# Kernel optimization log

Hardware: AMD Instinct MI355X
Metric: run time of the kernel (lower is better)

Reference implementation:

```python
import jax, jax.numpy as jnp
import numpy as np

B, T, E = 2, 2048, 1024
H, D = 16, 64          # num_heads, head_dim (v_head_dim == head_dim)


def setup_inputs() -> dict:
    key = jax.random.key(0)
    ks = jax.random.split(key, 10)
    s = lambda fan_in: 1.0 / np.sqrt(fan_in)
    inp = {
        "embed": jax.random.normal(ks[0], (B, T, E), dtype=jnp.float32),
        "mask": jax.random.randint(ks[1], (B, T, T), 0, 2) > 0,
        # Linear weights stored as [in, out] (y = x @ W + b)
        "Wq": jax.random.uniform(ks[2], (E, H * D), minval=-s(E), maxval=s(E)),
        "bq": jnp.zeros((H * D,), jnp.float32),
        "Wk": jax.random.uniform(ks[3], (E, H * D), minval=-s(E), maxval=s(E)),
        "bk": jnp.zeros((H * D,), jnp.float32),
        "Wv": jax.random.uniform(ks[4], (E, H * D), minval=-s(E), maxval=s(E)),
        "bv": jnp.zeros((H * D,), jnp.float32),
        "Wz": jax.random.uniform(ks[5], (H * D, E), minval=-s(H * D), maxval=s(H * D)),
        "bz": jnp.zeros((E,), jnp.float32),
    }
    return inp


def reference(embed, mask, Wq, bq, Wk, bk, Wv, bv, Wz, bz):
    # Self-attention: context = embed
    q = (embed @ Wq + bq).reshape(B, T, H, D)   # b t h d
    k = (embed @ Wk + bk).reshape(B, T, H, D)   # b T h d
    v = (embed @ Wv + bv).reshape(B, T, H, D)   # b T h d

    scale = D ** (-0.5)
    score = jnp.einsum('bthd,bThd->bhtT', q, k) * scale   # [b,h,t,T] materialized, as in source
    max_neg = -jnp.finfo(score.dtype).max
    score = jnp.where(mask[:, None, :, :], score, max_neg)
    norm_score = jax.nn.softmax(score, axis=-1)
    z = jnp.einsum('bhtT,bThd->bthd', norm_score, v)      # [b,t,h,d]
    flat_z = z.reshape(B, T, H * D)
    return flat_z @ Wz + bz
```

## Files before the change

### kernel.cpp

```cpp
#include <hip/hip_runtime.h>
#include <hip/hip_bf16.h>


typedef __bf16 bf8_t  __attribute__((ext_vector_type(8)));
typedef __bf16 bf4_t  __attribute__((ext_vector_type(4)));
typedef float  f4_t   __attribute__((ext_vector_type(4)));

constexpr int Bb = 2, Tt = 2048, Hh = 16, Dd = 64;

#define ASYNC16(g, l)                                                        \
    __builtin_amdgcn_global_load_lds(                                        \
        (const __attribute__((address_space(1))) void*)(g),                  \
        (__attribute__((address_space(3))) void*)(l), 16, 0, 0)

#if __has_builtin(__builtin_amdgcn_exp2f)
#define EXP2F(x) __builtin_amdgcn_exp2f(x)
#else
#define EXP2F(x) exp2f(x)
#endif

__global__ __launch_bounds__(256) void convert_kernel(
    const float* __restrict__ in, __bf16* __restrict__ out)
{
    int i = (blockIdx.x * 256 + threadIdx.x) * 4;
    float4 v = *reinterpret_cast<const float4*>(in + i);
    bf4_t o = {(__bf16)v.x, (__bf16)v.y, (__bf16)v.z, (__bf16)v.w};
    *reinterpret_cast<bf4_t*>(out + i) = o;
}

__global__ __launch_bounds__(256) void transpose_kernel(
    const float* __restrict__ w0, const float* __restrict__ w1,
    const float* __restrict__ w2, const float* __restrict__ w3,
    __bf16* __restrict__ o0, __bf16* __restrict__ o1,
    __bf16* __restrict__ o2, __bf16* __restrict__ o3)
{
    const float* in; __bf16* out;
    switch (blockIdx.z) {
        case 0: in = w0; out = o0; break;
        case 1: in = w1; out = o1; break;
        case 2: in = w2; out = o2; break;
        default: in = w3; out = o3; break;
    }
    __shared__ float t[32][33];
    int x  = threadIdx.x & 31;
    int y0 = threadIdx.x >> 5;
    int bx = blockIdx.x * 32;
    int by = blockIdx.y * 32;
    #pragma unroll
    for (int i = 0; i < 4; i++) {
        int y = y0 + i * 8;
        t[y][x] = in[(size_t)(by + y) * 1024 + bx + x];
    }
    __syncthreads();
    #pragma unroll
    for (int i = 0; i < 4; i++) {
        int y = y0 + i * 8;
        out[(size_t)(bx + y) * 1024 + by + x] = (__bf16)t[x][y];
    }
}

template <int TM, typename OutT>
__device__ __forceinline__ void gemm_body(const __bf16* __restrict__ A,
                                          const __bf16* __restrict__ Bt,
                                          const float* __restrict__ bias,
                                          OutT* __restrict__ out,
                                          int mode, float oscale, int bx, int by)
{
    constexpr int NI = TM / 32;
    alignas(16) __shared__ __bf16 As[TM * 64];
    alignas(16) __shared__ __bf16 Bs[128 * 64];

    int tid  = threadIdx.x;
    int lane = tid & 63;
    int quad = lane >> 4;
    int l16  = lane & 15;
    int wave = tid >> 6;
    int wm   = wave >> 1, wn = wave & 1;

    f4_t acc[NI][4];
    #pragma unroll
    for (int i = 0; i < NI; i++)
        #pragma unroll
        for (int j = 0; j < 4; j++)
            acc[i][j] = f4_t{0.f, 0.f, 0.f, 0.f};

    for (int kt = 0; kt < 1024; kt += 64) {
        #pragma unroll
        for (int i = 0; i < TM / 32; i++) {
            int c   = tid + 256 * i;
            int row = c >> 3, j = c & 7;
            ASYNC16(A + (size_t)(by * TM + row) * 1024 + kt + ((j ^ (row & 7)) * 8),
                    &As[c * 8]);
        }
        #pragma unroll
        for (int i = 0; i < 4; i++) {
            int c   = tid + 256 * i;
            int row = c >> 3, j = c & 7;
            ASYNC16(Bt + (size_t)(bx * 128 + row) * 1024 + kt + ((j ^ (row & 7)) * 8),
                    &Bs[c * 8]);
        }
        __syncthreads();

        bf8_t af[2][NI], bfr[2][4];
        #pragma unroll
        for (int c = 0; c < 2; c++) {
            #pragma unroll
            for (int im = 0; im < NI; im++) {
                int row = wm * (TM / 2) + im * 16 + l16;
                af[c][im] = *reinterpret_cast<const bf8_t*>(
                    &As[row * 64 + (((c * 4 + quad) ^ (row & 7)) * 8)]);
            }
            #pragma unroll
            for (int in_ = 0; in_ < 4; in_++) {
                int row = wn * 64 + in_ * 16 + l16;
                bfr[c][in_] = *reinterpret_cast<const bf8_t*>(
                    &Bs[row * 64 + (((c * 4 + quad) ^ (row & 7)) * 8)]);
            }
        }
        #pragma unroll
        for (int c = 0; c < 2; c++)
            #pragma unroll
            for (int im = 0; im < NI; im++)
                #pragma unroll
                for (int in_ = 0; in_ < 4; in_++)
                    acc[im][in_] = __builtin_amdgcn_mfma_f32_16x16x32_bf16(
                        af[c][im], bfr[c][in_], acc[im][in_], 0, 0, 0);
        __syncthreads();
    }

    #pragma unroll
    for (int im = 0; im < NI; im++) {
        #pragma unroll
        for (int in_ = 0; in_ < 4; in_++) {
            int gc  = bx * 128 + wn * 64 + in_ * 16 + l16;
            float bb = bias[gc];
            int gr0 = by * TM + wm * (TM / 2) + im * 16 + quad * 4;
            if (mode == 2) {
                int b = gr0 >> 11, t0 = gr0 & 2047;
                int h = gc >> 6,  d = gc & 63;
                bf4_t ov;
                #pragma unroll
                for (int r = 0; r < 4; r++)
                    ov[r] = (__bf16)(acc[im][in_][r] + bb);
                *reinterpret_cast<bf4_t*>(
                    (__bf16*)out + ((size_t)(b * Hh + h) * Dd + d) * Tt + t0) = ov;
            } else {
                #pragma unroll
                for (int r = 0; r < 4; r++) {
                    int gr  = gr0 + r;
                    float v = (acc[im][in_][r] + bb) * oscale;
                    size_t idx;
                    if (mode == 0) {
                        idx = (size_t)gr * 1024 + gc;
                    } else {
                        int b = gr >> 11, t = gr & 2047;
                        int h = gc >> 6,  d = gc & 63;
                        idx = ((size_t)(b * Hh + h) * Tt + t) * Dd + d;
                    }
                    out[idx] = (OutT)v;
                }
            }
        }
    }
}

__global__ __launch_bounds__(256) void gemm_qkv_kernel(
    const __bf16* __restrict__ A,
    const __bf16* __restrict__ WqT, const __bf16* __restrict__ WkT, const __bf16* __restrict__ WvT,
    const float* __restrict__ bq,  const float* __restrict__ bk,  const float* __restrict__ bv,
    __bf16* __restrict__ Qo, __bf16* __restrict__ Ko, __bf16* __restrict__ Vo)
{
    const __bf16* Bt; const float* bias; __bf16* out; int mode; float sc;
    if      (blockIdx.z == 0) { Bt = WqT; bias = bq; out = Qo; mode = 1; sc = 0.18033688011112042f; }
    else if (blockIdx.z == 1) { Bt = WkT; bias = bk; out = Ko; mode = 1; sc = 1.f; }
    else                      { Bt = WvT; bias = bv; out = Vo; mode = 2; sc = 1.f; }
    gemm_body<128, __bf16>(A, Bt, bias, out, mode, sc, blockIdx.x, blockIdx.y);
}

__global__ __launch_bounds__(256) void gemm_out_kernel(
    const __bf16* __restrict__ A, const __bf16* __restrict__ Bt,
    const float* __restrict__ bias, float* __restrict__ out)
{
    gemm_body<64, float>(A, Bt, bias, out, 0, 1.f, blockIdx.x, blockIdx.y);
}

__global__ __launch_bounds__(512, 4) void flash_kernel(
    const __bf16* __restrict__ Qb, const __bf16* __restrict__ Kb,
    const __bf16* __restrict__ Vb, const int* __restrict__ mask,
    __bf16* __restrict__ Zb)
{
    alignas(16) __shared__ __bf16 Ks[2][64 * 64];
    alignas(16) __shared__ __bf16 Vs[2][64 * 64];
    alignas(16) __shared__ __bf16 Ps[8 * 16 * 72];

    int tid  = threadIdx.x;
    int lane = tid & 63;
    int wave = tid >> 6;
    int quad = lane >> 4;
    int l16  = lane & 15;
    int b = blockIdx.z, h = blockIdx.y;
    int bh = b * Hh + h;
    int qrow = blockIdx.x * 128 + wave * 16;

    int srow = tid >> 3, sj = tid & 7;
    const __bf16* kgp = Kb + ((size_t)bh * Tt + srow) * Dd + ((sj ^ (srow & 7)) * 8);
    const __bf16* vgp = Vb + ((size_t)bh * Dd + srow) * Tt + ((sj ^ (srow & 7)) * 8);
    const int sdst = tid * 8;

    bf8_t qf[2];
    #pragma unroll
    for (int c = 0; c < 2; c++)
        qf[c] = *reinterpret_cast<const bf8_t*>(
            Qb + ((size_t)bh * Tt + qrow + l16) * Dd + c * 32 + quad * 8);

    const int* mp = mask + ((size_t)b * Tt + qrow + l16) * Tt + quad * 4;

    float l_i = 0.f;
    f4_t o[4];
    #pragma unroll
    for (int d = 0; d < 4; d++) o[d] = f4_t{0.f, 0.f, 0.f, 0.f};

    __bf16* pw = Ps + wave * 16 * 72;

    bf8_t kreg = *reinterpret_cast<const bf8_t*>(kgp);
    bf8_t vreg = *reinterpret_cast<const bf8_t*>(vgp);
    int4 ireg[4];
    #pragma unroll
    for (int n = 0; n < 4; n++)
        ireg[n] = *reinterpret_cast<const int4*>(mp + n * 16);

    for (int kt = 0; kt < Tt; kt += 64) {
        int par = (kt >> 6) & 1;
        *reinterpret_cast<bf8_t*>(&Ks[par][sdst]) = kreg;
        *reinterpret_cast<bf8_t*>(&Vs[par][sdst]) = vreg;
        f4_t s[4];
        #pragma unroll
        for (int n = 0; n < 4; n++)
            s[n] = f4_t{ireg[n].x ? 0.f : -1e30f, ireg[n].y ? 0.f : -1e30f,
                        ireg[n].z ? 0.f : -1e30f, ireg[n].w ? 0.f : -1e30f};
        __syncthreads();

        int ktn = (kt + 64 < Tt) ? kt + 64 : 0;
        kreg = *reinterpret_cast<const bf8_t*>(kgp + (size_t)ktn * Dd);
        vreg = *reinterpret_cast<const bf8_t*>(vgp + ktn);
        #pragma unroll
        for (int n = 0; n < 4; n++)
            ireg[n] = *reinterpret_cast<const int4*>(mp + ktn + n * 16);

        #pragma unroll
        for (int c = 0; c < 2; c++)
            #pragma unroll
            for (int n = 0; n < 4; n++) {
                int krow = n * 16 + l16;
                bf8_t kf = *reinterpret_cast<const bf8_t*>(
                    &Ks[par][krow * 64 + (((c * 4 + quad) ^ (krow & 7)) * 8)]);
                s[n] = __builtin_amdgcn_mfma_f32_16x16x32_bf16(kf, qf[c], s[n], 0, 0, 0);
            }

        float rs = 0.f;
        #pragma unroll
        for (int n = 0; n < 4; n++) {
            bf4_t pv4;
            #pragma unroll
            for (int r = 0; r < 4; r++) {
                float p = EXP2F(s[n][r]);
                rs += p;
                pv4[r] = (__bf16)p;
            }
            *reinterpret_cast<bf4_t*>(&pw[l16 * 72 + n * 16 + quad * 4]) = pv4;
        }
        rs += __shfl_xor(rs, 16);
        rs += __shfl_xor(rs, 32);
        l_i += rs;

        #pragma unroll
        for (int c = 0; c < 2; c++) {
            bf8_t pf = *reinterpret_cast<const bf8_t*>(
                &pw[l16 * 72 + c * 32 + quad * 8]);
            #pragma unroll
            for (int ds = 0; ds < 4; ds++) {
                int vrow = ds * 16 + l16;
                bf8_t vf = *reinterpret_cast<const bf8_t*>(
                    &Vs[par][vrow * 64 + (((c * 4 + quad) ^ (vrow & 7)) * 8)]);
                o[ds] = __builtin_amdgcn_mfma_f32_16x16x32_bf16(vf, pf, o[ds], 0, 0, 0);
            }
        }
    }

    float inv = 1.f / fmaxf(l_i, 1e-30f);
    size_t zrow = ((size_t)b * Tt + qrow + l16) * 1024 + h * 64;
    #pragma unroll
    for (int ds = 0; ds < 4; ds++) {
        bf4_t ov;
        #pragma unroll
        for (int r = 0; r < 4; r++) ov[r] = (__bf16)(o[ds][r] * inv);
        *reinterpret_cast<bf4_t*>(Zb + zrow + ds * 16 + quad * 4) = ov;
    }
}

extern "C" void kernel_launch(void* const* d_in, const int* in_sizes, int n_in,
                              void* d_out, int out_size, void* d_ws, size_t ws_size,
                              hipStream_t stream)
{
    (void)in_sizes; (void)n_in; (void)out_size; (void)ws_size;

    const float* embed = (const float*)d_in[0];
    const int*   mask  = (const int*)d_in[1];
    const float* Wq = (const float*)d_in[2];
    const float* bq = (const float*)d_in[3];
    const float* Wk = (const float*)d_in[4];
    const float* bk = (const float*)d_in[5];
    const float* Wv = (const float*)d_in[6];
    const float* bv = (const float*)d_in[7];
    const float* Wz = (const float*)d_in[8];
    const float* bz = (const float*)d_in[9];
    float* out = (float*)d_out;

    char* ws = (char*)d_ws;
    const size_t MB = (size_t)1024 * 1024;
    __bf16* WqT = (__bf16*)(ws + 0 * MB);
    __bf16* WkT = (__bf16*)(ws + 2 * MB);
    __bf16* WvT = (__bf16*)(ws + 4 * MB);
    __bf16* WzT = (__bf16*)(ws + 6 * MB);
    __bf16* Eb  = (__bf16*)(ws + 8 * MB);
    __bf16* Qb  = (__bf16*)(ws + 16 * MB);
    __bf16* Kb  = (__bf16*)(ws + 24 * MB);
    __bf16* Vb  = (__bf16*)(ws + 32 * MB);
    __bf16* Zb  = (__bf16*)(ws + 40 * MB);

    convert_kernel<<<dim3(4096), 256, 0, stream>>>(embed, Eb);
    transpose_kernel<<<dim3(32, 32, 4), 256, 0, stream>>>(Wq, Wk, Wv, Wz,
                                                          WqT, WkT, WvT, WzT);
    gemm_qkv_kernel<<<dim3(8, 32, 3), 256, 0, stream>>>(Eb, WqT, WkT, WvT,
                                                        bq, bk, bv, Qb, Kb, Vb);
    flash_kernel<<<dim3(16, Hh, Bb), 512, 0, stream>>>(Qb, Kb, Vb, mask, Zb);
    gemm_out_kernel<<<dim3(8, 64, 1), 256, 0, stream>>>(Zb, WzT, bz, out);
}
```

Before: 238.2 us.

## Process two query tiles per wave in flash attention to reuse K/V fragments

The flash kernel now runs 4 waves per block instead of 8, with each wave handling 32 query rows as two 16-row groups. Each K and V fragment read from LDS is reused for two MFMAs, halving LDS fragment traffic per unit of compute. The mask bias is also converted to bf16 at load time, so it is held in fewer registers. The trade-off is more accumulator registers per wave and fewer waves per block to hide latency.

```diff
diff --git a/kernel.cpp b/kernel.cpp
--- a/kernel.cpp
+++ b/kernel.cpp
@@ -184,14 +184,14 @@
     gemm_body<64, float>(A, Bt, bias, out, 0, 1.f, blockIdx.x, blockIdx.y);
 }
 
-__global__ __launch_bounds__(512, 4) void flash_kernel(
+__global__ __launch_bounds__(256, 2) void flash_kernel(
     const __bf16* __restrict__ Qb, const __bf16* __restrict__ Kb,
     const __bf16* __restrict__ Vb, const int* __restrict__ mask,
     __bf16* __restrict__ Zb)
 {
     alignas(16) __shared__ __bf16 Ks[2][64 * 64];
     alignas(16) __shared__ __bf16 Vs[2][64 * 64];
-    alignas(16) __shared__ __bf16 Ps[8 * 16 * 72];
+    alignas(16) __shared__ __bf16 Ps[4 * 2 * 16 * 72];
 
     int tid  = threadIdx.x;
     int lane = tid & 63;
@@ -200,52 +200,78 @@
     int l16  = lane & 15;
     int b = blockIdx.z, h = blockIdx.y;
     int bh = b * Hh + h;
-    int qrow = blockIdx.x * 128 + wave * 16;
-
-    int srow = tid >> 3, sj = tid & 7;
-    const __bf16* kgp = Kb + ((size_t)bh * Tt + srow) * Dd + ((sj ^ (srow & 7)) * 8);
-    const __bf16* vgp = Vb + ((size_t)bh * Dd + srow) * Tt + ((sj ^ (srow & 7)) * 8);
-    const int sdst = tid * 8;
-
-    bf8_t qf[2];
-    #pragma unroll
-    for (int c = 0; c < 2; c++)
-        qf[c] = *reinterpret_cast<const bf8_t*>(
-            Qb + ((size_t)bh * Tt + qrow + l16) * Dd + c * 32 + quad * 8);
-
-    const int* mp = mask + ((size_t)b * Tt + qrow + l16) * Tt + quad * 4;
-
-    float l_i = 0.f;
-    f4_t o[4];
-    #pragma unroll
-    for (int d = 0; d < 4; d++) o[d] = f4_t{0.f, 0.f, 0.f, 0.f};
-
-    __bf16* pw = Ps + wave * 16 * 72;
-
-    bf8_t kreg = *reinterpret_cast<const bf8_t*>(kgp);
-    bf8_t vreg = *reinterpret_cast<const bf8_t*>(vgp);
-    int4 ireg[4];
-    #pragma unroll
-    for (int n = 0; n < 4; n++)
-        ireg[n] = *reinterpret_cast<const int4*>(mp + n * 16);
+    int qbase = blockIdx.x * 128 + wave * 32;
+
+    int r0 = tid >> 3,        j0 = tid & 7;
+    int r1 = (tid + 256) >> 3, j1 = tid & 7;
+    const __bf16* kgp0 = Kb + ((size_t)bh * Tt + r0) * Dd + ((j0 ^ (r0 & 7)) * 8);
+    const __bf16* kgp1 = Kb + ((size_t)bh * Tt + r1) * Dd + ((j1 ^ (r1 & 7)) * 8);
+    const __bf16* vgp0 = Vb + ((size_t)bh * Dd + r0) * Tt + ((j0 ^ (r0 & 7)) * 8);
+    const __bf16* vgp1 = Vb + ((size_t)bh * Dd + r1) * Tt + ((j1 ^ (r1 & 7)) * 8);
+
+    bf8_t qf[2][2];
+    #pragma unroll
+    for (int qg = 0; qg < 2; qg++)
+        #pragma unroll
+        for (int c = 0; c < 2; c++)
+            qf[qg][c] = *reinterpret_cast<const bf8_t*>(
+                Qb + ((size_t)bh * Tt + qbase + qg * 16 + l16) * Dd + c * 32 + quad * 8);
+
+    const int* mp0 = mask + ((size_t)b * Tt + qbase + l16) * Tt + quad * 4;
+    const int* mp1 = mp0 + (size_t)16 * Tt;
+
+    float l_i[2] = {0.f, 0.f};
+    f4_t o[2][4];
+    #pragma unroll
+    for (int qg = 0; qg < 2; qg++)
+        #pragma unroll
+        for (int d = 0; d < 4; d++) o[qg][d] = f4_t{0.f, 0.f, 0.f, 0.f};
+
+    __bf16* pw0 = Ps + (wave * 2 + 0) * 16 * 72;
+    __bf16* pw1 = Ps + (wave * 2 + 1) * 16 * 72;
+
+    bf8_t kreg0 = *reinterpret_cast<const bf8_t*>(kgp0);
+    bf8_t kreg1 = *reinterpret_cast<const bf8_t*>(kgp1);
+    bf8_t vreg0 = *reinterpret_cast<const bf8_t*>(vgp0);
+    bf8_t vreg1 = *reinterpret_cast<const bf8_t*>(vgp1);
+    bf4_t breg[2][4];
+    #pragma unroll
+    for (int n = 0; n < 4; n++) {
+        int4 i0 = *reinterpret_cast<const int4*>(mp0 + n * 16);
+        int4 i1 = *reinterpret_cast<const int4*>(mp1 + n * 16);
+        const __bf16 z = (__bf16)0.f, neg = (__bf16)(-1e30f);
+        breg[0][n] = bf4_t{i0.x ? z : neg, i0.y ? z : neg, i0.z ? z : neg, i0.w ? z : neg};
+        breg[1][n] = bf4_t{i1.x ? z : neg, i1.y ? z : neg, i1.z ? z : neg, i1.w ? z : neg};
+    }
 
     for (int kt = 0; kt < Tt; kt += 64) {
         int par = (kt >> 6) & 1;
-        *reinterpret_cast<bf8_t*>(&Ks[par][sdst]) = kreg;
-        *reinterpret_cast<bf8_t*>(&Vs[par][sdst]) = vreg;
-        f4_t s[4];
-        #pragma unroll
-        for (int n = 0; n < 4; n++)
-            s[n] = f4_t{ireg[n].x ? 0.f : -1e30f, ireg[n].y ? 0.f : -1e30f,
-                        ireg[n].z ? 0.f : -1e30f, ireg[n].w ? 0.f : -1e30f};
+        *reinterpret_cast<bf8_t*>(&Ks[par][tid * 8])         = kreg0;
+        *reinterpret_cast<bf8_t*>(&Ks[par][(tid + 256) * 8]) = kreg1;
+        *reinterpret_cast<bf8_t*>(&Vs[par][tid * 8])         = vreg0;
+        *reinterpret_cast<bf8_t*>(&Vs[par][(tid + 256) * 8]) = vreg1;
+        f4_t s[2][4];
+        #pragma unroll
+        for (int qg = 0; qg < 2; qg++)
+            #pragma unroll
+            for (int n = 0; n < 4; n++)
+                s[qg][n] = f4_t{(float)breg[qg][n][0], (float)breg[qg][n][1],
+                                (float)breg[qg][n][2], (float)breg[qg][n][3]};
         __syncthreads();
 
         int ktn = (kt + 64 < Tt) ? kt + 64 : 0;
-        kreg = *reinterpret_cast<const bf8_t*>(kgp + (size_t)ktn * Dd);
-        vreg = *reinterpret_cast<const bf8_t*>(vgp + ktn);
-        #pragma unroll
-        for (int n = 0; n < 4; n++)
-            ireg[n] = *reinterpret_cast<const int4*>(mp + ktn + n * 16);
+        kreg0 = *reinterpret_cast<const bf8_t*>(kgp0 + (size_t)ktn * Dd);
+        kreg1 = *reinterpret_cast<const bf8_t*>(kgp1 + (size_t)ktn * Dd);
+        vreg0 = *reinterpret_cast<const bf8_t*>(vgp0 + ktn);
+        vreg1 = *reinterpret_cast<const bf8_t*>(vgp1 + ktn);
+        #pragma unroll
+        for (int n = 0; n < 4; n++) {
+            int4 i0 = *reinterpret_cast<const int4*>(mp0 + ktn + n * 16);
+            int4 i1 = *reinterpret_cast<const int4*>(mp1 + ktn + n * 16);
+            const __bf16 z = (__bf16)0.f, neg = (__bf16)(-1e30f);
+            breg[0][n] = bf4_t{i0.x ? z : neg, i0.y ? z : neg, i0.z ? z : neg, i0.w ? z : neg};
+            breg[1][n] = bf4_t{i1.x ? z : neg, i1.y ? z : neg, i1.z ? z : neg, i1.w ? z : neg};
+        }
 
         #pragma unroll
         for (int c = 0; c < 2; c++)
@@ -254,47 +280,56 @@
                 int krow = n * 16 + l16;
                 bf8_t kf = *reinterpret_cast<const bf8_t*>(
                     &Ks[par][krow * 64 + (((c * 4 + quad) ^ (krow & 7)) * 8)]);
-                s[n] = __builtin_amdgcn_mfma_f32_16x16x32_bf16(kf, qf[c], s[n], 0, 0, 0);
-            }
-
-        float rs = 0.f;
-        #pragma unroll
-        for (int n = 0; n < 4; n++) {
-            bf4_t pv4;
-            #pragma unroll
-            for (int r = 0; r < 4; r++) {
-                float p = EXP2F(s[n][r]);
-                rs += p;
-                pv4[r] = (__bf16)p;
-            }
-            *reinterpret_cast<bf4_t*>(&pw[l16 * 72 + n * 16 + quad * 4]) = pv4;
-        }
-        rs += __shfl_xor(rs, 16);
-        rs += __shfl_xor(rs, 32);
-        l_i += rs;
+                s[0][n] = __builtin_amdgcn_mfma_f32_16x16x32_bf16(kf, qf[0][c], s[0][n], 0, 0, 0);
+                s[1][n] = __builtin_amdgcn_mfma_f32_16x16x32_bf16(kf, qf[1][c], s[1][n], 0, 0, 0);
+            }
+
+        #pragma unroll
+        for (int qg = 0; qg < 2; qg++) {
+            __bf16* pw = qg ? pw1 : pw0;
+            float rs = 0.f;
+            #pragma unroll
+            for (int n = 0; n < 4; n++) {
+                bf4_t pv4;
+                #pragma unroll
+                for (int r = 0; r < 4; r++) {
+                    float p = EXP2F(s[qg][n][r]);
+                    rs += p;
+                    pv4[r] = (__bf16)p;
+                }
+                *reinterpret_cast<bf4_t*>(&pw[l16 * 72 + n * 16 + quad * 4]) = pv4;
+            }
+            rs += __shfl_xor(rs, 16);
+            rs += __shfl_xor(rs, 32);
+            l_i[qg] += rs;
+        }
 
         #pragma unroll
         for (int c = 0; c < 2; c++) {
-            bf8_t pf = *reinterpret_cast<const bf8_t*>(
-                &pw[l16 * 72 + c * 32 + quad * 8]);
+            bf8_t pf0 = *reinterpret_cast<const bf8_t*>(&pw0[l16 * 72 + c * 32 + quad * 8]);
+            bf8_t pf1 = *reinterpret_cast<const bf8_t*>(&pw1[l16 * 72 + c * 32 + quad * 8]);
             #pragma unroll
             for (int ds = 0; ds < 4; ds++) {
                 int vrow = ds * 16 + l16;
                 bf8_t vf = *reinterpret_cast<const bf8_t*>(
                     &Vs[par][vrow * 64 + (((c * 4 + quad) ^ (vrow & 7)) * 8)]);
-                o[ds] = __builtin_amdgcn_mfma_f32_16x16x32_bf16(vf, pf, o[ds], 0, 0, 0);
-            }
-        }
-    }
-
-    float inv = 1.f / fmaxf(l_i, 1e-30f);
-    size_t zrow = ((size_t)b * Tt + qrow + l16) * 1024 + h * 64;
-    #pragma unroll
-    for (int ds = 0; ds < 4; ds++) {
-        bf4_t ov;
-        #pragma unroll
-        for (int r = 0; r < 4; r++) ov[r] = (__bf16)(o[ds][r] * inv);
-        *reinterpret_cast<bf4_t*>(Zb + zrow + ds * 16 + quad * 4) = ov;
+                o[0][ds] = __builtin_amdgcn_mfma_f32_16x16x32_bf16(vf, pf0, o[0][ds], 0, 0, 0);
+                o[1][ds] = __builtin_amdgcn_mfma_f32_16x16x32_bf16(vf, pf1, o[1][ds], 0, 0, 0);
+            }
+        }
+    }
+
+    #pragma unroll
+    for (int qg = 0; qg < 2; qg++) {
+        float inv = 1.f / fmaxf(l_i[qg], 1e-30f);
+        size_t zrow = ((size_t)b * Tt + qbase + qg * 16 + l16) * 1024 + h * 64;
+        #pragma unroll
+        for (int ds = 0; ds < 4; ds++) {
+            bf4_t ov;
+            #pragma unroll
+            for (int r = 0; r < 4; r++) ov[r] = (__bf16)(o[qg][ds][r] * inv);
+            *reinterpret_cast<bf4_t*>(Zb + zrow + ds * 16 + quad * 4) = ov;
+        }
     }
 }
 
@@ -333,6 +368,6 @@
                                                           WqT, WkT, WvT, WzT);
     gemm_qkv_kernel<<<dim3(8, 32, 3), 256, 0, stream>>>(Eb, WqT, WkT, WvT,
                                                         bq, bk, bv, Qb, Kb, Vb);
-    flash_kernel<<<dim3(16, Hh, Bb), 512, 0, stream>>>(Qb, Kb, Vb, mask, Zb);
+    flash_kernel<<<dim3(16, Hh, Bb), 256, 0, stream>>>(Qb, Kb, Vb, mask, Zb);
     gemm_out_kernel<<<dim3(8, 64, 1), 256, 0, stream>>>(Zb, WzT, bz, out);
 }
```

After: 298.9 us. 25.5% more time.

## Split flash attention over two key halves and combine partials

Applied to the files above, without the earlier changes.

Splits the key/value sequence into two halves handled by separate blocks, which doubles the flash grid from 512 to 1024 blocks. Each block writes unnormalized fp32 partial outputs and row sums, and a new combine kernel adds them and normalizes into bf16. The occupancy hint rises to 6 blocks per CU. The aim is better CU utilization on the 256-CU device. The cost is an extra kernel launch plus roughly 32MB of fp32 partial writes and reads. Combining without a max correction is valid only because the scores carry no running-max subtraction (Q is pre-scaled and exp2 is used directly).

```diff
diff --git a/kernel.cpp b/kernel.cpp
--- a/kernel.cpp
+++ b/kernel.cpp
@@ -184,10 +184,10 @@
     gemm_body<64, float>(A, Bt, bias, out, 0, 1.f, blockIdx.x, blockIdx.y);
 }
 
-__global__ __launch_bounds__(512, 4) void flash_kernel(
+__global__ __launch_bounds__(512, 6) void flash_kernel(
     const __bf16* __restrict__ Qb, const __bf16* __restrict__ Kb,
     const __bf16* __restrict__ Vb, const int* __restrict__ mask,
-    __bf16* __restrict__ Zb)
+    float* __restrict__ Opart, float* __restrict__ Lpart)
 {
     alignas(16) __shared__ __bf16 Ks[2][64 * 64];
     alignas(16) __shared__ __bf16 Vs[2][64 * 64];
@@ -198,13 +198,16 @@
     int wave = tid >> 6;
     int quad = lane >> 4;
     int l16  = lane & 15;
-    int b = blockIdx.z, h = blockIdx.y;
-    int bh = b * Hh + h;
+    int b    = blockIdx.z >> 1;
+    int split= blockIdx.z & 1;
+    int h    = blockIdx.y;
+    int bh   = b * Hh + h;
     int qrow = blockIdx.x * 128 + wave * 16;
+    const int kt0 = split * 1024;
 
     int srow = tid >> 3, sj = tid & 7;
-    const __bf16* kgp = Kb + ((size_t)bh * Tt + srow) * Dd + ((sj ^ (srow & 7)) * 8);
-    const __bf16* vgp = Vb + ((size_t)bh * Dd + srow) * Tt + ((sj ^ (srow & 7)) * 8);
+    const __bf16* kgp = Kb + ((size_t)bh * Tt + kt0 + srow) * Dd + ((sj ^ (srow & 7)) * 8);
+    const __bf16* vgp = Vb + ((size_t)bh * Dd + srow) * Tt + kt0 + ((sj ^ (srow & 7)) * 8);
     const int sdst = tid * 8;
 
     bf8_t qf[2];
@@ -213,7 +216,7 @@
         qf[c] = *reinterpret_cast<const bf8_t*>(
             Qb + ((size_t)bh * Tt + qrow + l16) * Dd + c * 32 + quad * 8);
 
-    const int* mp = mask + ((size_t)b * Tt + qrow + l16) * Tt + quad * 4;
+    const int* mp = mask + ((size_t)b * Tt + qrow + l16) * Tt + kt0 + quad * 4;
 
     float l_i = 0.f;
     f4_t o[4];
@@ -229,7 +232,7 @@
     for (int n = 0; n < 4; n++)
         ireg[n] = *reinterpret_cast<const int4*>(mp + n * 16);
 
-    for (int kt = 0; kt < Tt; kt += 64) {
+    for (int kt = 0; kt < 1024; kt += 64) {
         int par = (kt >> 6) & 1;
         *reinterpret_cast<bf8_t*>(&Ks[par][sdst]) = kreg;
         *reinterpret_cast<bf8_t*>(&Vs[par][sdst]) = vreg;
@@ -240,7 +243,7 @@
                         ireg[n].z ? 0.f : -1e30f, ireg[n].w ? 0.f : -1e30f};
         __syncthreads();
 
-        int ktn = (kt + 64 < Tt) ? kt + 64 : 0;
+        int ktn = (kt + 64 < 1024) ? kt + 64 : 0;
         kreg = *reinterpret_cast<const bf8_t*>(kgp + (size_t)ktn * Dd);
         vreg = *reinterpret_cast<const bf8_t*>(vgp + ktn);
         #pragma unroll
@@ -287,15 +290,30 @@
         }
     }
 
-    float inv = 1.f / fmaxf(l_i, 1e-30f);
-    size_t zrow = ((size_t)b * Tt + qrow + l16) * 1024 + h * 64;
-    #pragma unroll
-    for (int ds = 0; ds < 4; ds++) {
-        bf4_t ov;
-        #pragma unroll
-        for (int r = 0; r < 4; r++) ov[r] = (__bf16)(o[ds][r] * inv);
-        *reinterpret_cast<bf4_t*>(Zb + zrow + ds * 16 + quad * 4) = ov;
-    }
+    size_t orow = ((size_t)(split * Bb + b) * Tt + qrow + l16) * 1024 + h * 64;
+    #pragma unroll
+    for (int ds = 0; ds < 4; ds++)
+        *reinterpret_cast<f4_t*>(Opart + orow + ds * 16 + quad * 4) = o[ds];
+    if (quad == 0)
+        Lpart[((size_t)(split * Bb + b) * Tt + qrow + l16) * Hh + h] = l_i;
+}
+
+__global__ __launch_bounds__(256) void combine_kernel(
+    const float* __restrict__ Opart, const float* __restrict__ Lpart,
+    __bf16* __restrict__ Zb)
+{
+    const size_t NTOT = (size_t)Bb * Tt * 1024;
+    size_t i = ((size_t)blockIdx.x * 256 + threadIdx.x) * 4;
+    size_t row = i >> 10;
+    int    h   = (int)((i & 1023) >> 6);
+    f4_t a = *reinterpret_cast<const f4_t*>(Opart + i);
+    f4_t c = *reinterpret_cast<const f4_t*>(Opart + NTOT + i);
+    float l = Lpart[row * Hh + h] + Lpart[(size_t)Bb * Tt * Hh + row * Hh + h];
+    float inv = 1.f / fmaxf(l, 1e-30f);
+    bf4_t ov;
+    #pragma unroll
+    for (int r = 0; r < 4; r++) ov[r] = (__bf16)((a[r] + c[r]) * inv);
+    *reinterpret_cast<bf4_t*>(Zb + i) = ov;
 }
 
 extern "C" void kernel_launch(void* const* d_in, const int* in_sizes, int n_in,
@@ -327,12 +345,15 @@
     __bf16* Kb  = (__bf16*)(ws + 24 * MB);
     __bf16* Vb  = (__bf16*)(ws + 32 * MB);
     __bf16* Zb  = (__bf16*)(ws + 40 * MB);
+    float*  Op  = (float*)(ws + 64 * MB);
+    float*  Lp  = (float*)(ws + 96 * MB);
 
     convert_kernel<<<dim3(4096), 256, 0, stream>>>(embed, Eb);
     transpose_kernel<<<dim3(32, 32, 4), 256, 0, stream>>>(Wq, Wk, Wv, Wz,
                                                           WqT, WkT, WvT, WzT);
     gemm_qkv_kernel<<<dim3(8, 32, 3), 256, 0, stream>>>(Eb, WqT, WkT, WvT,
                                                         bq, bk, bv, Qb, Kb, Vb);
-    flash_kernel<<<dim3(16, Hh, Bb), 512, 0, stream>>>(Qb, Kb, Vb, mask, Zb);
+    flash_kernel<<<dim3(16, Hh, Bb * 2), 512, 0, stream>>>(Qb, Kb, Vb, mask, Op, Lp);
+    combine_kernel<<<dim3(4096), 256, 0, stream>>>(Op, Lp, Zb);
     gemm_out_kernel<<<dim3(8, 64, 1), 256, 0, stream>>>(Zb, WzT, bz, out);
 }
```

Result: slower. 250.0 us (+4.9%).

## Fuse embed conversion into QKV GEMM and register-prefetch double-buffered GEMM tiles

Applied to the files above, without the earlier changes.

Removes the separate fp32->bf16 conversion kernel for the embeddings; the QKV GEMM now reads fp32 embed directly and converts in registers while staging to LDS. Both GEMMs switch from async global->LDS loads with two barriers per k-step to a register-prefetch scheme with double-buffered shared memory and one barrier per step, issuing the next tile's global loads before the MFMA work. Launch bounds now request two blocks per SM. In exchange, the QKV GEMM reads twice as many bytes of A per tile, uses more registers for the prefetch buffers, and doubles LDS use.

```diff
diff --git a/kernel.cpp b/kernel.cpp
--- a/kernel.cpp
+++ b/kernel.cpp
@@ -7,26 +7,12 @@
 typedef float  f4_t   __attribute__((ext_vector_type(4)));
 
 constexpr int Bb = 2, Tt = 2048, Hh = 16, Dd = 64;
-
-#define ASYNC16(g, l)                                                        \
-    __builtin_amdgcn_global_load_lds(                                        \
-        (const __attribute__((address_space(1))) void*)(g),                  \
-        (__attribute__((address_space(3))) void*)(l), 16, 0, 0)
 
 #if __has_builtin(__builtin_amdgcn_exp2f)
 #define EXP2F(x) __builtin_amdgcn_exp2f(x)
 #else
 #define EXP2F(x) exp2f(x)
 #endif
-
-__global__ __launch_bounds__(256) void convert_kernel(
-    const float* __restrict__ in, __bf16* __restrict__ out)
-{
-    int i = (blockIdx.x * 256 + threadIdx.x) * 4;
-    float4 v = *reinterpret_cast<const float4*>(in + i);
-    bf4_t o = {(__bf16)v.x, (__bf16)v.y, (__bf16)v.z, (__bf16)v.w};
-    *reinterpret_cast<bf4_t*>(out + i) = o;
-}
 
 __global__ __launch_bounds__(256) void transpose_kernel(
     const float* __restrict__ w0, const float* __restrict__ w1,
@@ -59,16 +45,20 @@
     }
 }
 
-template <int TM, typename OutT>
-__device__ __forceinline__ void gemm_body(const __bf16* __restrict__ A,
+template <int TM, bool AF32, typename OutT>
+__device__ __forceinline__ void gemm_dbuf(const void* __restrict__ Ap,
                                           const __bf16* __restrict__ Bt,
                                           const float* __restrict__ bias,
                                           OutT* __restrict__ out,
                                           int mode, float oscale, int bx, int by)
 {
+    constexpr int NA = TM / 32;
     constexpr int NI = TM / 32;
-    alignas(16) __shared__ __bf16 As[TM * 64];
-    alignas(16) __shared__ __bf16 Bs[128 * 64];
+    alignas(16) __shared__ __bf16 As[2][TM * 64];
+    alignas(16) __shared__ __bf16 Bs[2][128 * 64];
+
+    const float*  Af = (const float*)Ap;
+    const __bf16* Ab = (const __bf16*)Ap;
 
     int tid  = threadIdx.x;
     int lane = tid & 63;
@@ -77,6 +67,10 @@
     int wave = tid >> 6;
     int wm   = wave >> 1, wn = wave & 1;
 
+    const int srow = tid >> 3;
+    const int co   = (((tid & 7) ^ (srow & 7)) * 8);
+    const int sdst = tid * 8;
+
     f4_t acc[NI][4];
     #pragma unroll
     for (int i = 0; i < NI; i++)
@@ -84,22 +78,60 @@
         for (int j = 0; j < 4; j++)
             acc[i][j] = f4_t{0.f, 0.f, 0.f, 0.f};
 
+    float4 arf[NA][2];
+    bf8_t  arb[NA];
+    bf8_t  brg[4];
+
+    #pragma unroll
+    for (int i = 0; i < NA; i++) {
+        size_t off = (size_t)(by * TM + srow + 32 * i) * 1024 + co;
+        if constexpr (AF32) {
+            arf[i][0] = *reinterpret_cast<const float4*>(Af + off);
+            arf[i][1] = *reinterpret_cast<const float4*>(Af + off + 4);
+        } else {
+            arb[i] = *reinterpret_cast<const bf8_t*>(Ab + off);
+        }
+    }
+    #pragma unroll
+    for (int i = 0; i < 4; i++)
+        brg[i] = *reinterpret_cast<const bf8_t*>(
+            Bt + (size_t)(bx * 128 + srow + 32 * i) * 1024 + co);
+
     for (int kt = 0; kt < 1024; kt += 64) {
-        #pragma unroll
-        for (int i = 0; i < TM / 32; i++) {
-            int c   = tid + 256 * i;
-            int row = c >> 3, j = c & 7;
-            ASYNC16(A + (size_t)(by * TM + row) * 1024 + kt + ((j ^ (row & 7)) * 8),
-                    &As[c * 8]);
-        }
-        #pragma unroll
-        for (int i = 0; i < 4; i++) {
-            int c   = tid + 256 * i;
-            int row = c >> 3, j = c & 7;
-            ASYNC16(Bt + (size_t)(bx * 128 + row) * 1024 + kt + ((j ^ (row & 7)) * 8),
-                    &Bs[c * 8]);
-        }
+        int par = (kt >> 6) & 1;
+        #pragma unroll
+        for (int i = 0; i < NA; i++) {
+            bf8_t w;
+            if constexpr (AF32) {
+                w[0] = (__bf16)arf[i][0].x; w[1] = (__bf16)arf[i][0].y;
+                w[2] = (__bf16)arf[i][0].z; w[3] = (__bf16)arf[i][0].w;
+                w[4] = (__bf16)arf[i][1].x; w[5] = (__bf16)arf[i][1].y;
+                w[6] = (__bf16)arf[i][1].z; w[7] = (__bf16)arf[i][1].w;
+            } else {
+                w = arb[i];
+            }
+            *reinterpret_cast<bf8_t*>(&As[par][sdst + 2048 * i]) = w;
+        }
+        #pragma unroll
+        for (int i = 0; i < 4; i++)
+            *reinterpret_cast<bf8_t*>(&Bs[par][sdst + 2048 * i]) = brg[i];
         __syncthreads();
+
+        int ktn = (kt + 64 < 1024) ? kt + 64 : 0;
+        #pragma unroll
+        for (int i = 0; i < NA; i++) {
+            size_t off = (size_t)(by * TM + srow + 32 * i) * 1024 + ktn + co;
+            if constexpr (AF32) {
+                arf[i][0] = *reinterpret_cast<const float4*>(Af + off);
+                arf[i][1] = *reinterpret_cast<const float4*>(Af + off + 4);
+            } else {
+                arb[i] = *reinterpret_cast<const bf8_t*>(Ab + off);
+            }
+        }
+        #pragma unroll
+        for (int i = 0; i < 4; i++)
+            brg[i] = *reinterpret_cast<const bf8_t*>(
+                Bt + (size_t)(bx * 128 + srow + 32 * i) * 1024 + ktn + co);
 
         bf8_t af[2][NI], bfr[2][4];
         #pragma unroll
@@ -108,13 +140,13 @@
             for (int im = 0; im < NI; im++) {
                 int row = wm * (TM / 2) + im * 16 + l16;
                 af[c][im] = *reinterpret_cast<const bf8_t*>(
-                    &As[row * 64 + (((c * 4 + quad) ^ (row & 7)) * 8)]);
+                    &As[par][row * 64 + (((c * 4 + quad) ^ (row & 7)) * 8)]);
             }
             #pragma unroll
             for (int in_ = 0; in_ < 4; in_++) {
                 int row = wn * 64 + in_ * 16 + l16;
                 bfr[c][in_] = *reinterpret_cast<const bf8_t*>(
-                    &Bs[row * 64 + (((c * 4 + quad) ^ (row & 7)) * 8)]);
+                    &Bs[par][row * 64 + (((c * 4 + quad) ^ (row & 7)) * 8)]);
             }
         }
         #pragma unroll
@@ -125,7 +157,6 @@
                 for (int in_ = 0; in_ < 4; in_++)
                     acc[im][in_] = __builtin_amdgcn_mfma_f32_16x16x32_bf16(
                         af[c][im], bfr[c][in_], acc[im][in_], 0, 0, 0);
-        __syncthreads();
     }
 
     #pragma unroll
@@ -164,8 +195,8 @@
     }
 }
 
-__global__ __launch_bounds__(256) void gemm_qkv_kernel(
-    const __bf16* __restrict__ A,
+__global__ __launch_bounds__(256, 2) void gemm_qkv_kernel(
+    const float* __restrict__ A,
     const __bf16* __restrict__ WqT, const __bf16* __restrict__ WkT, const __bf16* __restrict__ WvT,
     const float* __restrict__ bq,  const float* __restrict__ bk,  const float* __restrict__ bv,
     __bf16* __restrict__ Qo, __bf16* __restrict__ Ko, __bf16* __restrict__ Vo)
@@ -174,14 +205,14 @@
     if      (blockIdx.z == 0) { Bt = WqT; bias = bq; out = Qo; mode = 1; sc = 0.18033688011112042f; }
     else if (blockIdx.z == 1) { Bt = WkT; bias = bk; out = Ko; mode = 1; sc = 1.f; }
     else                      { Bt = WvT; bias = bv; out = Vo; mode = 2; sc = 1.f; }
-    gemm_body<128, __bf16>(A, Bt, bias, out, mode, sc, blockIdx.x, blockIdx.y);
-}
-
-__global__ __launch_bounds__(256) void gemm_out_kernel(
+    gemm_dbuf<128, true, __bf16>(A, Bt, bias, out, mode, sc, blockIdx.x, blockIdx.y);
+}
+
+__global__ __launch_bounds__(256, 2) void gemm_out_kernel(
     const __bf16* __restrict__ A, const __bf16* __restrict__ Bt,
     const float* __restrict__ bias, float* __restrict__ out)
 {
-    gemm_body<64, float>(A, Bt, bias, out, 0, 1.f, blockIdx.x, blockIdx.y);
+    gemm_dbuf<64, false, float>(A, Bt, bias, out, 0, 1.f, blockIdx.x, blockIdx.y);
 }
 
 __global__ __launch_bounds__(512, 4) void flash_kernel(
@@ -322,16 +353,14 @@
     __bf16* WkT = (__bf16*)(ws + 2 * MB);
     __bf16* WvT = (__bf16*)(ws + 4 * MB);
     __bf16* WzT = (__bf16*)(ws + 6 * MB);
-    __bf16* Eb  = (__bf16*)(ws + 8 * MB);
     __bf16* Qb  = (__bf16*)(ws + 16 * MB);
     __bf16* Kb  = (__bf16*)(ws + 24 * MB);
     __bf16* Vb  = (__bf16*)(ws + 32 * MB);
     __bf16* Zb  = (__bf16*)(ws + 40 * MB);
 
-    convert_kernel<<<dim3(4096), 256, 0, stream>>>(embed, Eb);
     transpose_kernel<<<dim3(32, 32, 4), 256, 0, stream>>>(Wq, Wk, Wv, Wz,
                                                           WqT, WkT, WvT, WzT);
-    gemm_qkv_kernel<<<dim3(8, 32, 3), 256, 0, stream>>>(Eb, WqT, WkT, WvT,
+    gemm_qkv_kernel<<<dim3(8, 32, 3), 256, 0, stream>>>(embed, WqT, WkT, WvT,
                                                         bq, bk, bv, Qb, Kb, Vb);
     flash_kernel<<<dim3(16, Hh, Bb), 512, 0, stream>>>(Qb, Kb, Vb, mask, Zb);
     gemm_out_kernel<<<dim3(8, 64, 1), 256, 0, stream>>>(Zb, WzT, bz, out);
```

Result: slower. 258.6 us (+8.6%).
